# Kernel optimization log

Measured on AMD Instinct MI355X. Metric: run time of the kernel, lower is better.

## Reference

```python
import jax, jax.numpy as jnp
import numpy as np

B, T, C, HS = 8, 2048, 768, 256  # batch, seq(block_size), n_embed, head_size


def setup_inputs() -> dict:
    key = jax.random.key(0)
    kx, kq, kk, kv = jax.random.split(key, 4)
    scale = 1.0 / np.sqrt(C)
    return {
        "x": jax.random.normal(kx, (B, T, C), dtype=jnp.float32),
        # torch nn.Linear(n_embed, head_size, bias=False) computes x @ W.T;
        # store weights pre-transposed as [in, out].
        "Wq": jax.random.normal(kq, (C, HS), dtype=jnp.float32) * scale,
        "Wk": jax.random.normal(kk, (C, HS), dtype=jnp.float32) * scale,
        "Wv": jax.random.normal(kv, (C, HS), dtype=jnp.float32) * scale,
    }


def reference(x, Wq, Wk, Wv):
    Bx, Tx, Cx = x.shape
    q = x @ Wq  # [B,T,HS]
    k = x @ Wk  # [B,T,HS]
    v = x @ Wv  # [B,T,HS]
    # NOTE: original scales by C**-0.5 with C = n_embed (not head_size)
    att = jnp.einsum('btd,bsd->bts', q, k) * (Cx ** -0.5)  # [B,T,T]
    causal = jnp.tril(jnp.ones((Tx, Tx), dtype=bool))
    att = jnp.where(causal, att, -jnp.inf)
    probs = jax.nn.softmax(att, axis=-1)
    # dropout=0.0 -> identity (eval mode)
    out = jnp.einsum('bts,bsd->btd', probs, v)  # [B,T,HS]
    return out
```

## Files before the change

### kernel.cpp

```cpp
#include <hip/hip_runtime.h>
#include <hip/hip_bf16.h>
#include <math.h>

#define B_  8
#define T_  2048
#define C_  768
#define HS_ 256

#define CHUNKS_PER_BATCH 144
#define NSLOT (CHUNKS_PER_BATCH * B_)

typedef float  f32x4  __attribute__((ext_vector_type(4)));
typedef __bf16 bf16x8 __attribute__((ext_vector_type(8)));
typedef __bf16 bf16x4 __attribute__((ext_vector_type(4)));
typedef __bf16 bf16x2 __attribute__((ext_vector_type(2)));

#define MFMA16(a, b, c) __builtin_amdgcn_mfma_f32_16x16x32_bf16((a), (b), (c), 0, 0, 0)

#define GLOAD_LDS16(gp, lp)                                                     \
    __builtin_amdgcn_global_load_lds(                                           \
        (const __attribute__((address_space(1))) void*)(gp),                    \
        (__attribute__((address_space(3))) void*)(lp), 16, 0, 0)

__device__ __forceinline__ int chunk_cum64(int qb) {
    int g = qb >> 2;
    return 2 * g * (g + 1) + (qb & 3) * (g + 1);
}

__global__ __launch_bounds__(256) void xb_kernel(const float* __restrict__ x,
                                                 __bf16* __restrict__ xb) {
    size_t i = ((size_t)blockIdx.x * 256 + threadIdx.x) * 8;
    f32x4 a = *(const f32x4*)(x + i);
    f32x4 b = *(const f32x4*)(x + i + 4);
    bf16x8 o;
    o[0] = (__bf16)a[0]; o[1] = (__bf16)a[1]; o[2] = (__bf16)a[2]; o[3] = (__bf16)a[3];
    o[4] = (__bf16)b[0]; o[5] = (__bf16)b[1]; o[6] = (__bf16)b[2]; o[7] = (__bf16)b[3];
    *(bf16x8*)(xb + i) = o;
}

__global__ __launch_bounds__(256) void wt_kernel(const float* __restrict__ Wq,
                                                 const float* __restrict__ Wk,
                                                 const float* __restrict__ Wv,
                                                 __bf16* __restrict__ wt_all,
                                                 float qscale) {
    int idx = blockIdx.x * 256 + threadIdx.x;
    int mat = blockIdx.y;
    const float* W = (mat == 0) ? Wq : ((mat == 1) ? Wk : Wv);
    float scale = (mat == 0) ? qscale : 1.0f;
    int k = idx >> 8;
    int n = idx & 255;
    wt_all[((size_t)mat * HS_ + n) * C_ + k] = (__bf16)(W[idx] * scale);
}

__global__ __launch_bounds__(256) void proj_kernel(const __bf16* __restrict__ xb,
                                                   const __bf16* __restrict__ wt,
                                                   __bf16* __restrict__ qf_,
                                                   __bf16* __restrict__ kf_,
                                                   __bf16* __restrict__ vf_) {
    __shared__ alignas(16) __bf16 ldsA[128 * 64];
    __shared__ alignas(16) __bf16 ldsB[128 * 64];

    const int tid  = threadIdx.x;
    const int w    = tid >> 6;
    const int lane = tid & 63;
    const int cm   = lane & 15;
    const int quad = lane >> 4;
    const int wm   = w & 1;
    const int wn   = w >> 1;
    const int m0   = blockIdx.x * 128;
    const int n0   = blockIdx.y * 128;
    const int mat  = n0 >> 8;

    f32x4 acc[4][4];
#pragma unroll
    for (int i = 0; i < 4; i++)
#pragma unroll
        for (int j = 0; j < 4; j++) acc[i][j] = (f32x4){0.f, 0.f, 0.f, 0.f};

    if (mat < 2) {
        for (int k0 = 0; k0 < C_; k0 += 64) {
            __syncthreads();
#pragma unroll
            for (int h = 0; h < 4; h++) {
                int c = tid + h * 256;
                GLOAD_LDS16(xb + (size_t)(m0 + (c >> 3)) * C_ + k0 + (c & 7) * 8,
                            ldsA + c * 8);
            }
#pragma unroll
            for (int h = 0; h < 4; h++) {
                int c = tid + h * 256;
                GLOAD_LDS16(wt + (size_t)(n0 + (c >> 3)) * C_ + k0 + (c & 7) * 8,
                            ldsB + c * 8);
            }
            __syncthreads();

#pragma unroll
            for (int ks = 0; ks < 2; ks++) {
                bf16x8 af[4], bfr[4];
#pragma unroll
                for (int mt = 0; mt < 4; mt++)
                    af[mt] = *(const bf16x8*)&ldsA[(wm * 64 + mt * 16 + cm) * 64 + ks * 32 + quad * 8];
#pragma unroll
                for (int nt = 0; nt < 4; nt++)
                    bfr[nt] = *(const bf16x8*)&ldsB[(wn * 64 + nt * 16 + cm) * 64 + ks * 32 + quad * 8];
#pragma unroll
                for (int dt = 0; dt < 4; dt++)
#pragma unroll
                    for (int qt2 = 0; qt2 < 4; qt2++)
                        acc[dt][qt2] = MFMA16(bfr[dt], af[qt2], acc[dt][qt2]);
            }
        }
        const int dBase = (n0 & 255) + wn * 64;
        const int b     = m0 >> 11;
        const int rt2   = ((m0 & 2047) >> 6) + wm;
        __bf16* dst = (mat == 0) ? qf_ : kf_;
#pragma unroll
        for (int dt = 0; dt < 4; dt++)
#pragma unroll
            for (int qt2 = 0; qt2 < 4; qt2++) {
                int d0    = dBase + dt * 16 + quad * 4;
                int ksq   = d0 >> 5;
                int quadp = (d0 >> 3) & 3;
                int j0    = d0 & 7;
                size_t addr;
                if (mat == 0)
                    addr = ((((size_t)(b * 32 + rt2) * 4 + qt2) * 8 + ksq) * 64
                            + quadp * 16 + cm) * 8 + j0;
                else
                    addr = ((((size_t)(b * 32 + rt2) * 8 + ksq) * 4 + qt2) * 64
                            + quadp * 16 + cm) * 8 + j0;
                bf16x4 v4;
                v4[0] = (__bf16)acc[dt][qt2][0]; v4[1] = (__bf16)acc[dt][qt2][1];
                v4[2] = (__bf16)acc[dt][qt2][2]; v4[3] = (__bf16)acc[dt][qt2][3];
                *(bf16x4*)(dst + addr) = v4;
            }
    } else {
        for (int k0 = 0; k0 < C_; k0 += 64) {
            __syncthreads();
#pragma unroll
            for (int h = 0; h < 4; h++) {
                int c = tid + h * 256;
                GLOAD_LDS16(xb + (size_t)(m0 + (c >> 3)) * C_ + k0 + (c & 7) * 8,
                            ldsA + c * 8);
            }
#pragma unroll
            for (int h = 0; h < 4; h++) {
                int c = tid + h * 256;
                GLOAD_LDS16(wt + (size_t)(n0 + (c >> 3)) * C_ + k0 + (c & 7) * 8,
                            ldsB + c * 8);
            }
            __syncthreads();

#pragma unroll
            for (int ks = 0; ks < 2; ks++) {
                bf16x8 af[4], bfr[4];
#pragma unroll
                for (int mt = 0; mt < 4; mt++)
                    af[mt] = *(const bf16x8*)&ldsA[(wm * 64 + mt * 16 + cm) * 64 + ks * 32 + quad * 8];
#pragma unroll
                for (int nt = 0; nt < 4; nt++)
                    bfr[nt] = *(const bf16x8*)&ldsB[(wn * 64 + nt * 16 + cm) * 64 + ks * 32 + quad * 8];
#pragma unroll
                for (int mt = 0; mt < 4; mt++)
#pragma unroll
                    for (int nt = 0; nt < 4; nt++)
                        acc[mt][nt] = MFMA16(af[mt], bfr[nt], acc[mt][nt]);
            }
        }
        const int dBase = (n0 & 255) + wn * 64;
        const int b     = m0 >> 11;
        const int rt    = ((m0 & 2047) + wm * 64) >> 6;
#pragma unroll
        for (int mt = 0; mt < 4; mt++) {
            int ks2   = (mt >> 1) & 1;
            int quadF = (mt & 1) * 2 + (quad >> 1);
            int jb    = (quad & 1) * 4;
#pragma unroll
            for (int nt = 0; nt < 4; nt++) {
                int ntv = (dBase >> 4) + nt;
                size_t idx = ((((size_t)(b * 32 + rt) * 2 + ks2) * 16 + ntv) * 64
                              + quadF * 16 + cm) * 8 + jb;
                bf16x4 v4;
                v4[0] = (__bf16)acc[mt][nt][0]; v4[1] = (__bf16)acc[mt][nt][1];
                v4[2] = (__bf16)acc[mt][nt][2]; v4[3] = (__bf16)acc[mt][nt][3];
                *(bf16x4*)(vf_ + idx) = v4;
            }
        }
    }
}

__global__ __launch_bounds__(256) void flash_part(const __bf16* __restrict__ qf_,
                                                  const __bf16* __restrict__ kf_,
                                                  const __bf16* __restrict__ vf_,
                                                  __bf16* __restrict__ Opart,
                                                  float* __restrict__ mpart,
                                                  float* __restrict__ lpart) {
    __shared__ alignas(16) __bf16 ldsK[8 * 2 * 64 * 8];
    __shared__ alignas(16) __bf16 ldsV[16 * 64 * 8];
    __shared__ alignas(16) __bf16 ldsP[4][512];

    const int tid  = threadIdx.x;
    const int w    = tid >> 6;
    const int lane = tid & 63;
    const int cm   = lane & 15;
    const int quad = lane >> 4;

    const int pid  = blockIdx.x;
    const int b    = pid & 7;
    const int r    = (CHUNKS_PER_BATCH - 1) - (pid >> 3);
    int qb = 0, ci = 0;
    {
        int rr = r;
        for (int j = 0; j < 32; j++) {
            int c = (j >> 2) + 1;
            if (rr < c) { qb = j; ci = rr; break; }
            rr -= c;
        }
    }
    const int lpid = b * CHUNKS_PER_BATCH + r;
    const int kt_begin = ci * 8;
    const int kt_end   = min(kt_begin + 8, 2 * qb + 2);

    const __bf16* qp = qf_ + (((size_t)(b * 32 + qb) * 4 + w) * 8) * 512 + lane * 8;
    bf16x8 qf[8];
#pragma unroll
    for (int ks = 0; ks < 8; ks++) qf[ks] = *(const bf16x8*)(qp + ks * 512);

    f32x4 accO[16];
#pragma unroll
    for (int i = 0; i < 16; i++) accO[i] = (f32x4){0.f, 0.f, 0.f, 0.f};
    float mi = -__builtin_inff(), li = 0.f;

    const int wrow  = qb * 64 + w * 16;
    const int qglob = wrow + cm;

    for (int kt = kt_begin; kt < kt_end; kt++) {
        __syncthreads();

        {
            const int kt64 = kt >> 1, kh = kt & 1;
            const __bf16* kgb = kf_ + (((size_t)(b * 32 + kt64) * 8) * 4 + kh * 2) * 512;
#pragma unroll
            for (int h = 0; h < 4; h++) {
                int g = h * 256 + tid;
                int ks = g >> 7, sub = g & 127;
                GLOAD_LDS16(kgb + (size_t)ks * 4 * 512 + sub * 8,
                            ldsK + (h * 256 + w * 64) * 8);
            }
            const __bf16* vgb = vf_ + ((size_t)(b * 64 + kt) * 16) * 512;
#pragma unroll
            for (int h = 0; h < 4; h++) {
                int g = h * 256 + tid;
                GLOAD_LDS16(vgb + (size_t)g * 8,
                            ldsV + (h * 256 + w * 64) * 8);
            }
        }
        __syncthreads();

        f32x4 s[2];
#pragma unroll
        for (int i = 0; i < 2; i++) s[i] = (f32x4){0.f, 0.f, 0.f, 0.f};
#pragma unroll
        for (int ns = 0; ns < 2; ns++)
#pragma unroll
            for (int ks = 0; ks < 8; ks++) {
                bf16x8 kfr = *(const bf16x8*)&ldsK[(ks * 2 + ns) * 512 + lane * 8];
                s[ns] = MFMA16(kfr, qf[ks], s[ns]);
            }
        if (kt * 32 + 31 > wrow) {
#pragma unroll
            for (int ns = 0; ns < 2; ns++)
#pragma unroll
                for (int i = 0; i < 4; i++)
                    if (kt * 32 + ns * 16 + quad * 4 + i > qglob)
                        s[ns][i] = -__builtin_inff();
        }
        float pm = -__builtin_inff();
#pragma unroll
        for (int ns = 0; ns < 2; ns++)
#pragma unroll
            for (int i = 0; i < 4; i++) pm = fmaxf(pm, s[ns][i]);
        pm = fmaxf(pm, __shfl_xor(pm, 16));
        pm = fmaxf(pm, __shfl_xor(pm, 32));

        float mn = fmaxf(mi, pm);
        float al = exp2f(mi - mn);
        mi = mn;
        float p[2][4], rs = 0.f;
#pragma unroll
        for (int ns = 0; ns < 2; ns++)
#pragma unroll
            for (int i = 0; i < 4; i++) {
                p[ns][i] = exp2f(s[ns][i] - mn);
                rs += p[ns][i];
            }
        rs += __shfl_xor(rs, 16);
        rs += __shfl_xor(rs, 32);
        li = li * al + rs;

        if (__any(al != 1.0f)) {
            float aa[4];
#pragma unroll
            for (int i = 0; i < 4; i++) aa[i] = __shfl(al, quad * 4 + i);
#pragma unroll
            for (int nt = 0; nt < 16; nt++)
#pragma unroll
                for (int i = 0; i < 4; i++) accO[nt][i] *= aa[i];
        }

#pragma unroll
        for (int ns = 0; ns < 2; ns++)
#pragma unroll
            for (int i2 = 0; i2 < 2; i2++) {
                bf16x2 d2;
                d2[0] = (__bf16)p[ns][2 * i2];
                d2[1] = (__bf16)p[ns][2 * i2 + 1];
                int off = ((ns * 2 + (quad >> 1)) * 16 + cm) * 8
                          + (quad & 1) * 4 + i2 * 2;
                *(bf16x2*)&ldsP[w][off] = d2;
            }
        bf16x8 pfrag = *(const bf16x8*)&ldsP[w][(quad * 16 + cm) * 8];
#pragma unroll
        for (int nt = 0; nt < 16; nt++) {
            bf16x8 vfr = *(const bf16x8*)&ldsV[(nt * 64 + lane) * 8];
            accO[nt] = MFMA16(pfrag, vfr, accO[nt]);
        }
    }

#pragma unroll
    for (int nt = 0; nt < 16; nt++)
#pragma unroll
        for (int i = 0; i < 4; i++)
            Opart[((size_t)lpid * 64 + w * 16 + quad * 4 + i) * HS_ + nt * 16 + cm]
                = (__bf16)accO[nt][i];
    if (quad == 0) {
        mpart[lpid * 64 + w * 16 + cm] = mi;
        lpart[lpid * 64 + w * 16 + cm] = li;
    }
}

__global__ __launch_bounds__(256) void flash_combine(const __bf16* __restrict__ Opart,
                                                     const float* __restrict__ mpart,
                                                     const float* __restrict__ lpart,
                                                     float* __restrict__ out) {
    const int b    = blockIdx.x >> 5;
    const int qb   = blockIdx.x & 31;
    const int nc   = (qb >> 2) + 1;
    const int pid0 = b * CHUNKS_PER_BATCH + chunk_cum64(qb);

    const int tid  = threadIdx.x;
    const int col  = (tid & 63) * 4;
    const int r0   = blockIdx.y * 16 + (tid >> 6) * 4;

    f32x4 ms = (f32x4){-__builtin_inff(), -__builtin_inff(),
                       -__builtin_inff(), -__builtin_inff()};
    for (int c = 0; c < nc; c++) {
        f32x4 m4 = *(const f32x4*)(mpart + (pid0 + c) * 64 + r0);
#pragma unroll
        for (int i = 0; i < 4; i++) ms[i] = fmaxf(ms[i], m4[i]);
    }
    f32x4 acc[4];
#pragma unroll
    for (int i = 0; i < 4; i++) acc[i] = (f32x4){0.f, 0.f, 0.f, 0.f};
    f32x4 lt = (f32x4){0.f, 0.f, 0.f, 0.f};
    for (int c = 0; c < nc; c++) {
        f32x4 m4 = *(const f32x4*)(mpart + (pid0 + c) * 64 + r0);
        f32x4 l4 = *(const f32x4*)(lpart + (pid0 + c) * 64 + r0);
#pragma unroll
        for (int i = 0; i < 4; i++) {
            float sc = exp2f(m4[i] - ms[i]);
            lt[i] += l4[i] * sc;
            bf16x4 o = *(const bf16x4*)(Opart
                        + ((size_t)(pid0 + c) * 64 + r0 + i) * HS_ + col);
            acc[i][0] += (float)o[0] * sc; acc[i][1] += (float)o[1] * sc;
            acc[i][2] += (float)o[2] * sc; acc[i][3] += (float)o[3] * sc;
        }
    }
#pragma unroll
    for (int i = 0; i < 4; i++) {
        float inv = 1.0f / lt[i];
        f32x4 res = (f32x4){acc[i][0] * inv, acc[i][1] * inv,
                            acc[i][2] * inv, acc[i][3] * inv};
        *(f32x4*)(out + ((size_t)(b * T_ + qb * 64 + r0 + i)) * HS_ + col) = res;
    }
}

extern "C" void kernel_launch(void* const* d_in, const int* in_sizes, int n_in,
                              void* d_out, int out_size, void* d_ws, size_t ws_size,
                              hipStream_t stream) {
    const float* x  = (const float*)d_in[0];
    const float* Wq = (const float*)d_in[1];
    const float* Wk = (const float*)d_in[2];
    const float* Wv = (const float*)d_in[3];
    float* out = (float*)d_out;

    char* ws = (char*)d_ws;
    size_t off = 0;
    __bf16* wt_all = (__bf16*)(ws + off); off += 1179648;
    __bf16* qfrag  = (__bf16*)(ws + off); off += 8388608;
    __bf16* kfrag  = (__bf16*)(ws + off); off += 8388608;
    __bf16* vfrag  = (__bf16*)(ws + off); off += 8388608;
    __bf16* xb     = (__bf16*)(ws + off);
    __bf16* Opart  = (__bf16*)(ws + off); off += (size_t)NSLOT * 64 * HS_ * 2;
    float*  mpart  = (float*)(ws + off);  off += (size_t)NSLOT * 64 * 4;
    float*  lpart  = (float*)(ws + off);

    float qscale = 1.4426950408889634f / sqrtf((float)C_);

    xb_kernel<<<dim3(6144), 256, 0, stream>>>(x, xb);
    wt_kernel<<<dim3(768, 3), 256, 0, stream>>>(Wq, Wk, Wv, wt_all, qscale);
    proj_kernel<<<dim3(128, 6), 256, 0, stream>>>(xb, wt_all, qfrag, kfrag, vfrag);
    flash_part<<<dim3(NSLOT), 256, 0, stream>>>(qfrag, kfrag, vfrag, Opart, mpart, lpart);
    flash_combine<<<dim3(256, 4), 256, 0, stream>>>(Opart, mpart, lpart, out);
}
```

Measured before the change: 200.0 us.

## Merge prep kernels, double-buffer projection GEMM, transpose PV MFMA output

Merges the x cast and weight transpose into one prep launch, with the weight transpose now writing 8 bf16 per thread. Rewrites the projection GEMM loop to double-buffer 32-wide K tiles in LDS, so the next tile's global-to-LDS load overlaps the current tile's MFMAs and each step needs one barrier instead of two. In the flash kernel, swaps the MFMA operand order for P·V so each lane holds a row-contiguous output, which removes the alpha shuffles and allows vectorized bf16x4 stores to Opart. The cost is a smaller K step (more loop iterations) and a riskier single-barrier double-buffer scheme.

```diff
diff --git a/kernel.cpp b/kernel.cpp
--- a/kernel.cpp
+++ b/kernel.cpp
@@ -27,29 +27,36 @@
     return 2 * g * (g + 1) + (qb & 3) * (g + 1);
 }
 
-__global__ __launch_bounds__(256) void xb_kernel(const float* __restrict__ x,
-                                                 __bf16* __restrict__ xb) {
-    size_t i = ((size_t)blockIdx.x * 256 + threadIdx.x) * 8;
-    f32x4 a = *(const f32x4*)(x + i);
-    f32x4 b = *(const f32x4*)(x + i + 4);
-    bf16x8 o;
-    o[0] = (__bf16)a[0]; o[1] = (__bf16)a[1]; o[2] = (__bf16)a[2]; o[3] = (__bf16)a[3];
-    o[4] = (__bf16)b[0]; o[5] = (__bf16)b[1]; o[6] = (__bf16)b[2]; o[7] = (__bf16)b[3];
-    *(bf16x8*)(xb + i) = o;
-}
-
-__global__ __launch_bounds__(256) void wt_kernel(const float* __restrict__ Wq,
-                                                 const float* __restrict__ Wk,
-                                                 const float* __restrict__ Wv,
-                                                 __bf16* __restrict__ wt_all,
-                                                 float qscale) {
-    int idx = blockIdx.x * 256 + threadIdx.x;
-    int mat = blockIdx.y;
-    const float* W = (mat == 0) ? Wq : ((mat == 1) ? Wk : Wv);
-    float scale = (mat == 0) ? qscale : 1.0f;
-    int k = idx >> 8;
-    int n = idx & 255;
-    wt_all[((size_t)mat * HS_ + n) * C_ + k] = (__bf16)(W[idx] * scale);
+__global__ __launch_bounds__(256) void prep_kernel(const float* __restrict__ x,
+                                                   const float* __restrict__ Wq,
+                                                   const float* __restrict__ Wk,
+                                                   const float* __restrict__ Wv,
+                                                   __bf16* __restrict__ xb,
+                                                   __bf16* __restrict__ wt_all,
+                                                   float qscale) {
+    const int bid = blockIdx.x;
+    if (bid < 6144) {
+        size_t i = ((size_t)bid * 256 + threadIdx.x) * 8;
+        f32x4 a = *(const f32x4*)(x + i);
+        f32x4 b = *(const f32x4*)(x + i + 4);
+        bf16x8 o;
+        o[0] = (__bf16)a[0]; o[1] = (__bf16)a[1]; o[2] = (__bf16)a[2]; o[3] = (__bf16)a[3];
+        o[4] = (__bf16)b[0]; o[5] = (__bf16)b[1]; o[6] = (__bf16)b[2]; o[7] = (__bf16)b[3];
+        *(bf16x8*)(xb + i) = o;
+    } else {
+        int idx = (bid - 6144) * 256 + threadIdx.x;
+        int n   = idx & 255;
+        int t   = idx >> 8;
+        int mat = t / 96;
+        int k8  = t - mat * 96;
+        const float* W = (mat == 0) ? Wq : ((mat == 1) ? Wk : Wv);
+        float scale = (mat == 0) ? qscale : 1.0f;
+        bf16x8 o;
+#pragma unroll
+        for (int j = 0; j < 8; j++)
+            o[j] = (__bf16)(W[(k8 * 8 + j) * HS_ + n] * scale);
+        *(bf16x8*)&wt_all[((size_t)mat * HS_ + n) * C_ + k8 * 8] = o;
+    }
 }
 
 __global__ __launch_bounds__(256) void proj_kernel(const __bf16* __restrict__ xb,
@@ -57,8 +64,8 @@
                                                    __bf16* __restrict__ qf_,
                                                    __bf16* __restrict__ kf_,
                                                    __bf16* __restrict__ vf_) {
-    __shared__ alignas(16) __bf16 ldsA[128 * 64];
-    __shared__ alignas(16) __bf16 ldsB[128 * 64];
+    __shared__ alignas(16) __bf16 ldsA[2][128 * 32];
+    __shared__ alignas(16) __bf16 ldsB[2][128 * 32];
 
     const int tid  = threadIdx.x;
     const int w    = tid >> 6;
@@ -77,42 +84,55 @@
 #pragma unroll
         for (int j = 0; j < 4; j++) acc[i][j] = (f32x4){0.f, 0.f, 0.f, 0.f};
 
+#pragma unroll
+    for (int h = 0; h < 2; h++) {
+        int c = tid + h * 256;
+        GLOAD_LDS16(xb + (size_t)(m0 + (c >> 2)) * C_ + (c & 3) * 8, &ldsA[0][c * 8]);
+        GLOAD_LDS16(wt + (size_t)(n0 + (c >> 2)) * C_ + (c & 3) * 8, &ldsB[0][c * 8]);
+    }
+
+    for (int kt = 0; kt < 24; kt++) {
+        const int cur = kt & 1;
+        __syncthreads();
+
+        if (kt < 23) {
+            const int k0 = (kt + 1) * 32;
+#pragma unroll
+            for (int h = 0; h < 2; h++) {
+                int c = tid + h * 256;
+                GLOAD_LDS16(xb + (size_t)(m0 + (c >> 2)) * C_ + k0 + (c & 3) * 8,
+                            &ldsA[cur ^ 1][c * 8]);
+                GLOAD_LDS16(wt + (size_t)(n0 + (c >> 2)) * C_ + k0 + (c & 3) * 8,
+                            &ldsB[cur ^ 1][c * 8]);
+            }
+        }
+
+        bf16x8 af[4], bfr[4];
+#pragma unroll
+        for (int mt = 0; mt < 4; mt++)
+            af[mt] = *(const bf16x8*)&ldsA[cur][(wm * 64 + mt * 16 + cm) * 32 + quad * 8];
+#pragma unroll
+        for (int nt = 0; nt < 4; nt++)
+            bfr[nt] = *(const bf16x8*)&ldsB[cur][(wn * 64 + nt * 16 + cm) * 32 + quad * 8];
+        if (mat < 2) {
+#pragma unroll
+            for (int dt = 0; dt < 4; dt++)
+#pragma unroll
+                for (int qt2 = 0; qt2 < 4; qt2++)
+                    acc[dt][qt2] = MFMA16(bfr[dt], af[qt2], acc[dt][qt2]);
+        } else {
+#pragma unroll
+            for (int mt = 0; mt < 4; mt++)
+#pragma unroll
+                for (int nt = 0; nt < 4; nt++)
+                    acc[mt][nt] = MFMA16(af[mt], bfr[nt], acc[mt][nt]);
+        }
+    }
+
+    const int dBase = (n0 & 255) + wn * 64;
+    const int b     = m0 >> 11;
     if (mat < 2) {
-        for (int k0 = 0; k0 < C_; k0 += 64) {
-            __syncthreads();
-#pragma unroll
-            for (int h = 0; h < 4; h++) {
-                int c = tid + h * 256;
-                GLOAD_LDS16(xb + (size_t)(m0 + (c >> 3)) * C_ + k0 + (c & 7) * 8,
-                            ldsA + c * 8);
-            }
-#pragma unroll
-            for (int h = 0; h < 4; h++) {
-                int c = tid + h * 256;
-                GLOAD_LDS16(wt + (size_t)(n0 + (c >> 3)) * C_ + k0 + (c & 7) * 8,
-                            ldsB + c * 8);
-            }
-            __syncthreads();
-
-#pragma unroll
-            for (int ks = 0; ks < 2; ks++) {
-                bf16x8 af[4], bfr[4];
-#pragma unroll
-                for (int mt = 0; mt < 4; mt++)
-                    af[mt] = *(const bf16x8*)&ldsA[(wm * 64 + mt * 16 + cm) * 64 + ks * 32 + quad * 8];
-#pragma unroll
-                for (int nt = 0; nt < 4; nt++)
-                    bfr[nt] = *(const bf16x8*)&ldsB[(wn * 64 + nt * 16 + cm) * 64 + ks * 32 + quad * 8];
-#pragma unroll
-                for (int dt = 0; dt < 4; dt++)
-#pragma unroll
-                    for (int qt2 = 0; qt2 < 4; qt2++)
-                        acc[dt][qt2] = MFMA16(bfr[dt], af[qt2], acc[dt][qt2]);
-            }
-        }
-        const int dBase = (n0 & 255) + wn * 64;
-        const int b     = m0 >> 11;
-        const int rt2   = ((m0 & 2047) >> 6) + wm;
+        const int rt2 = ((m0 & 2047) >> 6) + wm;
         __bf16* dst = (mat == 0) ? qf_ : kf_;
 #pragma unroll
         for (int dt = 0; dt < 4; dt++)
@@ -135,41 +155,7 @@
                 *(bf16x4*)(dst + addr) = v4;
             }
     } else {
-        for (int k0 = 0; k0 < C_; k0 += 64) {
-            __syncthreads();
-#pragma unroll
-            for (int h = 0; h < 4; h++) {
-                int c = tid + h * 256;
-                GLOAD_LDS16(xb + (size_t)(m0 + (c >> 3)) * C_ + k0 + (c & 7) * 8,
-                            ldsA + c * 8);
-            }
-#pragma unroll
-            for (int h = 0; h < 4; h++) {
-                int c = tid + h * 256;
-                GLOAD_LDS16(wt + (size_t)(n0 + (c >> 3)) * C_ + k0 + (c & 7) * 8,
-                            ldsB + c * 8);
-            }
-            __syncthreads();
-
-#pragma unroll
-            for (int ks = 0; ks < 2; ks++) {
-                bf16x8 af[4], bfr[4];
-#pragma unroll
-                for (int mt = 0; mt < 4; mt++)
-                    af[mt] = *(const bf16x8*)&ldsA[(wm * 64 + mt * 16 + cm) * 64 + ks * 32 + quad * 8];
-#pragma unroll
-                for (int nt = 0; nt < 4; nt++)
-                    bfr[nt] = *(const bf16x8*)&ldsB[(wn * 64 + nt * 16 + cm) * 64 + ks * 32 + quad * 8];
-#pragma unroll
-                for (int mt = 0; mt < 4; mt++)
-#pragma unroll
-                    for (int nt = 0; nt < 4; nt++)
-                        acc[mt][nt] = MFMA16(af[mt], bfr[nt], acc[mt][nt]);
-            }
-        }
-        const int dBase = (n0 & 255) + wn * 64;
-        const int b     = m0 >> 11;
-        const int rt    = ((m0 & 2047) + wm * 64) >> 6;
+        const int rt = ((m0 & 2047) + wm * 64) >> 6;
 #pragma unroll
         for (int mt = 0; mt < 4; mt++) {
             int ks2   = (mt >> 1) & 1;
@@ -299,13 +285,10 @@
         li = li * al + rs;
 
         if (__any(al != 1.0f)) {
-            float aa[4];
-#pragma unroll
-            for (int i = 0; i < 4; i++) aa[i] = __shfl(al, quad * 4 + i);
 #pragma unroll
             for (int nt = 0; nt < 16; nt++)
 #pragma unroll
-                for (int i = 0; i < 4; i++) accO[nt][i] *= aa[i];
+                for (int i = 0; i < 4; i++) accO[nt][i] *= al;
         }
 
 #pragma unroll
@@ -323,16 +306,18 @@
 #pragma unroll
         for (int nt = 0; nt < 16; nt++) {
             bf16x8 vfr = *(const bf16x8*)&ldsV[(nt * 64 + lane) * 8];
-            accO[nt] = MFMA16(pfrag, vfr, accO[nt]);
-        }
-    }
-
-#pragma unroll
-    for (int nt = 0; nt < 16; nt++)
-#pragma unroll
-        for (int i = 0; i < 4; i++)
-            Opart[((size_t)lpid * 64 + w * 16 + quad * 4 + i) * HS_ + nt * 16 + cm]
-                = (__bf16)accO[nt][i];
+            accO[nt] = MFMA16(vfr, pfrag, accO[nt]);
+        }
+    }
+
+    __bf16* op = Opart + ((size_t)lpid * 64 + w * 16 + cm) * HS_;
+#pragma unroll
+    for (int nt = 0; nt < 16; nt++) {
+        bf16x4 v4;
+        v4[0] = (__bf16)accO[nt][0]; v4[1] = (__bf16)accO[nt][1];
+        v4[2] = (__bf16)accO[nt][2]; v4[3] = (__bf16)accO[nt][3];
+        *(bf16x4*)(op + nt * 16 + quad * 4) = v4;
+    }
     if (quad == 0) {
         mpart[lpid * 64 + w * 16 + cm] = mi;
         lpart[lpid * 64 + w * 16 + cm] = li;
@@ -407,8 +392,7 @@
 
     float qscale = 1.4426950408889634f / sqrtf((float)C_);
 
-    xb_kernel<<<dim3(6144), 256, 0, stream>>>(x, xb);
-    wt_kernel<<<dim3(768, 3), 256, 0, stream>>>(Wq, Wk, Wv, wt_all, qscale);
+    prep_kernel<<<dim3(6432), 256, 0, stream>>>(x, Wq, Wk, Wv, xb, wt_all, qscale);
     proj_kernel<<<dim3(128, 6), 256, 0, stream>>>(xb, wt_all, qfrag, kfrag, vfrag);
     flash_part<<<dim3(NSLOT), 256, 0, stream>>>(qfrag, kfrag, vfrag, Opart, mpart, lpart);
     flash_combine<<<dim3(256, 4), 256, 0, stream>>>(Opart, mpart, lpart, out);
```

New measurement: 192.0 us. 4.0% less time.
